# Performance work log

Hardware: AMD Instinct MI355X
Metric: run time of the kernel (lower is better)

Reference implementation:

```python
import jax, jax.numpy as jnp
from jax import lax
import numpy as np

B, C0, C1 = 4, 128, 256
HF = WF = 256
HC = WC = 128
N_CROPS = 2048
WS0, WS1 = 8, 10
PAD0, PAD1 = 0, 1
STRIDE = 8
NW = (WF + 2 * PAD0 - WS0) // STRIDE + 1  # 32 windows per row (same for both crops)


def setup_inputs() -> dict:
    key = jax.random.key(0)
    ks = jax.random.split(key, 16)
    inp = {
        'x0_fine': jax.random.normal(ks[0], (B, C0, HF, WF), jnp.float32),
        'x0_coarse': jax.random.normal(ks[1], (B, C1, HC, WC), jnp.float32),
        'x1_fine': jax.random.normal(ks[2], (B, C0, HF, WF), jnp.float32),
        'x1_coarse': jax.random.normal(ks[3], (B, C1, HC, WC), jnp.float32),
        'proj0_w': jax.random.normal(ks[4], (C1, C0, 1, 1), jnp.float32) * 0.05,
        'proj_last_w': jax.random.normal(ks[5], (C1, C1, 1, 1), jnp.float32) * 0.05,
        'fuse_w1': jax.random.normal(ks[6], (C1, C1, 3, 3), jnp.float32) * 0.02,
        'bn_gamma': jnp.ones((C1,), jnp.float32),
        'bn_beta': jnp.zeros((C1,), jnp.float32),
        'bn_mean': jax.random.normal(ks[7], (C1,), jnp.float32) * 0.1,
        'bn_var': jax.random.uniform(ks[8], (C1,), jnp.float32) + 0.5,
        'fuse_w2': jax.random.normal(ks[9], (C0, C1, 3, 3), jnp.float32) * 0.02,
        'b_idx': jax.random.randint(ks[10], (N_CROPS,), 0, B, jnp.int32),
        'i_idx': jax.random.randint(ks[11], (N_CROPS,), 0, NW * NW, jnp.int32),
        'j_idx': jax.random.randint(ks[12], (N_CROPS,), 0, NW * NW, jnp.int32),
    }
    return inp


def conv2d(x, w, pad):
    return lax.conv_general_dilated(x, w, (1, 1), [(pad, pad), (pad, pad)],
                                    dimension_numbers=('NCHW', 'OIHW', 'NCHW'))


def up2_align_corners(x):
    # bilinear upsample x2 with align_corners=True, separable along H then W
    def interp(x, axis):
        n_in = x.shape[axis]
        n_out = 2 * n_in
        pos = jnp.arange(n_out, dtype=x.dtype) * ((n_in - 1) / (n_out - 1))
        i0 = jnp.clip(jnp.floor(pos).astype(jnp.int32), 0, n_in - 2)
        w = pos - i0.astype(x.dtype)
        a = jnp.take(x, i0, axis=axis)
        b = jnp.take(x, i0 + 1, axis=axis)
        shp = [1] * x.ndim
        shp[axis] = n_out
        w = w.reshape(shp)
        return a * (1 - w) + b * w
    return interp(interp(x, 2), 3)


def fuse(fine, coarse, proj0_w, proj_last_w, fuse_w1, bn_gamma, bn_beta, bn_mean, bn_var, fuse_w2):
    x0 = conv2d(coarse, proj_last_w, 0)                 # projs[-1]
    x0 = conv2d(fine, proj0_w, 0) + up2_align_corners(x0)
    y = conv2d(x0, fuse_w1, 1)
    inv = lax.rsqrt(bn_var + 1e-5)
    y = (y - bn_mean[None, :, None, None]) * (bn_gamma * inv)[None, :, None, None] + bn_beta[None, :, None, None]
    y = jnp.where(y >= 0, y, 0.01 * y)                  # LeakyReLU
    return conv2d(y, fuse_w2, 1)


def crop_windows(x, ws, pad, b, idx):
    # direct sparse window gather; avoids materializing the dense unfold tensor
    xp = jnp.pad(x, ((0, 0), (0, 0), (pad, pad), (pad, pad)))
    nW = (x.shape[3] + 2 * pad - ws) // STRIDE + 1
    r0 = (idx // nW) * STRIDE
    c0 = (idx % nW) * STRIDE
    rows = r0[:, None] + jnp.arange(ws)                 # [n, ws]
    cols = c0[:, None] + jnp.arange(ws)                 # [n, ws]
    crops = xp[b[:, None, None], :, rows[:, :, None], cols[:, None, :]]  # [n, ws, ws, C]
    return jnp.transpose(crops, (0, 3, 1, 2))           # [n, C, ws, ws]


def reference(x0_fine, x0_coarse, x1_fine, x1_coarse, proj0_w, proj_last_w,
              fuse_w1, bn_gamma, bn_beta, bn_mean, bn_var, fuse_w2,
              b_idx, i_idx, j_idx):
    # shapes equal -> concat, fuse once, chunk (matches torch branch)
    fine = jnp.concatenate([x0_fine, x1_fine], 0)
    coarse = jnp.concatenate([x0_coarse, x1_coarse], 0)
    y = fuse(fine, coarse, proj0_w, proj_last_w, fuse_w1, bn_gamma, bn_beta, bn_mean, bn_var, fuse_w2)
    x0, x1 = y[:B], y[B:]
    x0_cropped = crop_windows(x0, WS0, PAD0, b_idx, i_idx)
    x1_cropped = crop_windows(x1, WS1, PAD1, b_idx, j_idx)
    return (x0_cropped, x1_cropped)
```

## Files before the change

kernel.cpp:

```cpp
#include <hip/hip_runtime.h>

typedef __attribute__((ext_vector_type(8))) __bf16 bf16x8;
typedef __attribute__((ext_vector_type(4))) float f32x4;
typedef __attribute__((ext_vector_type(16))) float f32x16;

__device__ __forceinline__ unsigned short fbf(float f) {
  union { float f; unsigned u; } x; x.f = f;
  unsigned r = x.u + 0x7fffu + ((x.u >> 16) & 1u);
  return (unsigned short)(r >> 16);
}
__device__ __forceinline__ float bf2f(unsigned short h) {
  union { unsigned u; float f; } x; x.u = ((unsigned)h) << 16;
  return x.f;
}

#define OFF_WPL 0u
#define OFF_WP0 131072u
#define OFF_WT1 196608u
#define OFF_WT2 1376256u
#define OFF_BNS 1966080u
#define OFF_BNB 1967104u
#define OFF_T1  4194304u
#define OFF_X0  (OFF_T1 + 67108864u)
#define OFF_Y   (OFF_X0 + 268435456u)
#define OFF_YF  OFF_T1

__global__ void prep_kernel(const float* __restrict__ pl, const float* __restrict__ p0,
                            const float* __restrict__ w1, const float* __restrict__ w2,
                            const float* __restrict__ gam, const float* __restrict__ bet,
                            const float* __restrict__ mean, const float* __restrict__ var,
                            unsigned short* __restrict__ wpl, unsigned short* __restrict__ wp0,
                            unsigned short* __restrict__ wt1, unsigned short* __restrict__ wt2,
                            float* __restrict__ bns, float* __restrict__ bnb) {
  int t = blockIdx.x * blockDim.x + threadIdx.x;
  int stride = gridDim.x * blockDim.x;
  for (int i = t; i < 65536; i += stride) wpl[i] = fbf(pl[i]);
  for (int i = t; i < 32768; i += stride) wp0[i] = fbf(p0[i]);
  for (int i = t; i < 589824; i += stride) {
    int e = i & 7, l = (i >> 3) & 63, ks = (i >> 9) & 1;
    int cib = (i >> 10) & 7, cb = (i >> 13) & 7, tap = i >> 16;
    int ci = cib * 32 + ks * 16 + (l >> 5) * 8 + e;
    int co = cb * 32 + (l & 31);
    wt1[i] = fbf(w1[(co * 256 + ci) * 9 + tap]);
  }
  for (int i = t; i < 294912; i += stride) {
    int e = i & 7, l = (i >> 3) & 63, ks = (i >> 9) & 1;
    int cib = (i >> 10) & 7, cb = (i >> 13) & 3, tap = i >> 15;
    int ci = cib * 32 + ks * 16 + (l >> 5) * 8 + e;
    int co = cb * 32 + (l & 31);
    wt2[i] = fbf(w2[(co * 256 + ci) * 9 + tap]);
  }
  for (int i = t; i < 256; i += stride) {
    float s = gam[i] * rsqrtf(var[i] + 1e-5f);
    bns[i] = s; bnb[i] = bet[i] - mean[i] * s;
  }
}

template <int K, int HW, int WD, int EPI>
__global__ __launch_bounds__(512) void gemm1x1_kernel(
    const float* __restrict__ srcA, const float* __restrict__ srcB,
    const unsigned short* __restrict__ wmat,
    unsigned short* __restrict__ outp,
    const unsigned short* __restrict__ t1) {
  __shared__ unsigned short in_lds[128 * 32];
  __shared__ unsigned short w_lds[128 * 32];
  const int tid = threadIdx.x;
  const int pix0 = blockIdx.x * 128;
  const int co0 = blockIdx.y * 128;
  const int n = pix0 / HW;
  const int rem = pix0 % HW;
  const int h = rem / WD;
  const int w0 = rem % WD;
  const float* src = (n < 4) ? (srcA + (size_t)n * K * HW) : (srcB + (size_t)(n - 4) * K * HW);
  const float* rowbase = src + (size_t)h * WD + w0;
  const int wv = tid >> 6, lane = tid & 63;
  const int pw = wv >> 1, cw = wv & 1;
  const int l15 = lane & 15, k8 = lane >> 4;
  f32x4 zero = {0.f, 0.f, 0.f, 0.f};
  f32x4 acc[2][4];
#pragma unroll
  for (int i = 0; i < 2; i++)
#pragma unroll
    for (int j = 0; j < 4; j++) acc[i][j] = zero;
  const int sci = tid >> 4;
  const int sps = (tid & 15) * 8;
  const int wrow = tid >> 2, wsg = tid & 3;
  for (int cib = 0; cib < K / 32; ++cib) {
    int ci0 = cib * 32;
    __syncthreads();
    {
      const float* p = rowbase + (size_t)(ci0 + sci) * HW + sps;
      float4 v0 = *(const float4*)p;
      float4 v1 = *(const float4*)(p + 4);
      float vv[8] = {v0.x, v0.y, v0.z, v0.w, v1.x, v1.y, v1.z, v1.w};
#pragma unroll
      for (int i = 0; i < 8; i++) {
        int row = sps + i;
        int g = (sci >> 3) ^ ((row >> 1) & 3);
        in_lds[row * 32 + g * 8 + (sci & 7)] = fbf(vv[i]);
      }
    }
    {
      int4 v = *(const int4*)&wmat[(size_t)(co0 + wrow) * K + ci0 + wsg * 8];
      *(int4*)&w_lds[wrow * 32 + ((wsg ^ ((wrow >> 1) & 3)) << 3)] = v;
    }
    __syncthreads();
    bf16x8 b[4];
#pragma unroll
    for (int nf = 0; nf < 4; nf++) {
      int row = cw * 64 + nf * 16 + l15;
      b[nf] = *(const bf16x8*)&w_lds[row * 32 + ((k8 ^ ((row >> 1) & 3)) << 3)];
    }
#pragma unroll
    for (int mf = 0; mf < 2; mf++) {
      int row = pw * 32 + mf * 16 + l15;
      bf16x8 a = *(const bf16x8*)&in_lds[row * 32 + ((k8 ^ ((row >> 1) & 3)) << 3)];
#pragma unroll
      for (int nf = 0; nf < 4; nf++)
        acc[mf][nf] = __builtin_amdgcn_mfma_f32_16x16x32_bf16(a, b[nf], acc[mf][nf], 0, 0, 0);
    }
  }
  float fh = 0.f; int i0 = 0;
  if (EPI == 1) {
    float ph = (float)h * (127.0f / 255.0f);
    i0 = (int)ph; if (i0 > 126) i0 = 126;
    fh = ph - (float)i0;
  }
#pragma unroll
  for (int mf = 0; mf < 2; mf++) {
#pragma unroll
    for (int nf = 0; nf < 4; nf++) {
      int co = co0 + cw * 64 + nf * 16 + l15;
#pragma unroll
      for (int r = 0; r < 4; r++) {
        int m = pw * 32 + mf * 16 + k8 * 4 + r;
        float v = acc[mf][nf][r];
        if (EPI == 1) {
          int ww = w0 + m;
          float pww = (float)ww * (127.0f / 255.0f);
          int j0 = (int)pww; if (j0 > 126) j0 = 126;
          float fw = pww - (float)j0;
          const unsigned short* tb = t1 + ((size_t)(n * 128 + i0) * 128 + j0) * 256 + co;
          float a00 = bf2f(tb[0]);
          float a01 = bf2f(tb[256]);
          float a10 = bf2f(tb[128 * 256]);
          float a11 = bf2f(tb[128 * 256 + 256]);
          float top = a00 + fw * (a01 - a00);
          float bot = a10 + fw * (a11 - a10);
          v += top + fh * (bot - top);
        }
        outp[(size_t)(pix0 + m) * 256 + co] = fbf(v);
      }
    }
  }
}

template <int COT, int BNRELU>
__global__ __launch_bounds__(256, 2) void conv3x3_kernel(
    const unsigned short* __restrict__ inp,
    const unsigned short* __restrict__ wtr,
    unsigned short* __restrict__ outp,
    const float* __restrict__ bns, const float* __restrict__ bnb) {
  constexpr int WPT = COT / 32;
  __shared__ unsigned short xl[2][4 * 204 * 8];
  const int tid = threadIdx.x;
  const int bx = blockIdx.x;
  const int n = bx >> 9;
  const int h0 = ((bx >> 3) & 63) * 4;
  const int w0 = (bx & 7) * 32;
  const int co0 = blockIdx.y * 128;
  const int lane = tid & 63, cw = tid >> 6;
  const int l31 = lane & 31, lh = lane >> 5;
  const int cb = (co0 >> 5) + cw;

  f32x16 acc[4];
#pragma unroll
  for (int m = 0; m < 4; m++)
#pragma unroll
    for (int r = 0; r < 16; r++) acc[m][r] = 0.f;

#define FRAG_ADDR(tap, ks, cc) ((((size_t)((tap) * WPT + cb) * 8 + (cc)) * 2 + (ks)) * 512 + lane * 8)

  bf16x8 B[3][3][2];
#pragma unroll
  for (int kh = 0; kh < 3; kh++)
#pragma unroll
    for (int kw = 0; kw < 3; kw++)
#pragma unroll
      for (int ks = 0; ks < 2; ks++)
        B[kh][kw][ks] = *(const bf16x8*)&wtr[FRAG_ADDR(kh * 3 + kw, ks, 0)];

  const size_t nbase = (size_t)n * 256 * 256 * 256;
  for (int s = tid; s < 816; s += 256) {
    int p = s >> 2, g = s & 3;
    int row = p / 34, col = p - row * 34;
    int gh = h0 + row - 1, gw = w0 + col - 1;
    int4 v = make_int4(0, 0, 0, 0);
    if ((unsigned)gh < 256u && (unsigned)gw < 256u)
      v = *(const int4*)&inp[nbase + ((size_t)gh * 256 + gw) * 256 + g * 8];
    *(int4*)&xl[0][(g * 204 + p) * 8] = v;
  }
  __syncthreads();

  for (int cib = 0; cib < 8; ++cib) {
    const int cin = (cib + 1) & 7;
    int4 vr[4]; bool va[4]; int ldst[4];
    if (cib < 7) {
#pragma unroll
      for (int q = 0; q < 4; ++q) {
        int s = tid + q * 256;
        va[q] = s < 816;
        int p = s >> 2, g = s & 3;
        int row = p / 34, col = p - row * 34;
        int gh = h0 + row - 1, gw = w0 + col - 1;
        ldst[q] = (g * 204 + p) * 8;
        vr[q] = make_int4(0, 0, 0, 0);
        if (va[q] && (unsigned)gh < 256u && (unsigned)gw < 256u)
          vr[q] = *(const int4*)&inp[nbase + ((size_t)gh * 256 + gw) * 256 + cin * 32 + g * 8];
      }
    }
    const unsigned short* xb = xl[cib & 1];
    bf16x8 af[2][6];
#pragma unroll
    for (int kw = 0; kw < 3; kw++)
#pragma unroll
      for (int ks = 0; ks < 2; ks++)
        af[0][kw * 2 + ks] = *(const bf16x8*)&xb[((ks * 2 + lh) * 204 + l31 + kw) * 8];
    __builtin_amdgcn_s_setprio(1);
#pragma unroll
    for (int r = 0; r < 6; ++r) {
      const int cur = r & 1, nxt = cur ^ 1;
      if (r < 5) {
#pragma unroll
        for (int kw = 0; kw < 3; kw++)
#pragma unroll
          for (int ks = 0; ks < 2; ks++)
            af[nxt][kw * 2 + ks] =
                *(const bf16x8*)&xb[((ks * 2 + lh) * 204 + (r + 1) * 34 + l31 + kw) * 8];
      }
#pragma unroll
      for (int kw = 0; kw < 3; kw++)
#pragma unroll
        for (int ks = 0; ks < 2; ks++)
#pragma unroll
          for (int kh = 0; kh < 3; kh++) {
            int m = r - kh;
            if (m >= 0 && m < 4)
              acc[m] = __builtin_amdgcn_mfma_f32_32x32x16_bf16(af[cur][kw * 2 + ks],
                                                               B[kh][kw][ks], acc[m], 0, 0, 0);
          }
      if (r >= 3) {
        int kh = r - 3;
#pragma unroll
        for (int kw = 0; kw < 3; ++kw)
#pragma unroll
          for (int ks = 0; ks < 2; ++ks)
            B[kh][kw][ks] = *(const bf16x8*)&wtr[FRAG_ADDR(kh * 3 + kw, ks, cin)];
      }
    }
    __builtin_amdgcn_s_setprio(0);
    if (cib < 7) {
#pragma unroll
      for (int q = 0; q < 4; ++q)
        if (va[q]) *(int4*)&xl[cin & 1][ldst[q]] = vr[q];
      __syncthreads();
    }
  }
#undef FRAG_ADDR

  const int coL = co0 + cw * 32 + l31;
  float s = 1.f, t = 0.f;
  if (BNRELU) { s = bns[coL]; t = bnb[coL]; }
#pragma unroll
  for (int m = 0; m < 4; ++m) {
    int h = h0 + m;
    size_t rowb = (((size_t)(n * 256 + h) * 256) + w0) * COT + coL;
#pragma unroll
    for (int r = 0; r < 16; ++r) {
      int wofs = (r & 3) + 8 * (r >> 2) + 4 * lh;
      float v = acc[m][r];
      if (BNRELU) { v = v * s + t; v = (v >= 0.f) ? v : 0.01f * v; }
      outp[rowb + (size_t)wofs * COT] = fbf(v);
    }
  }
}

template <int WS, int PAD>
__global__ __launch_bounds__(256) void gather_kernel(
    const unsigned short* __restrict__ yf,
    const int* __restrict__ bidx, const int* __restrict__ widx,
    int bofs, float* __restrict__ outp) {
  const int WS2 = WS * WS;
  __shared__ unsigned short tile[WS * WS * 140];
  const int crop = blockIdx.x, tid = threadIdx.x;
  const int b = bidx[crop] + bofs;
  const int idx = widx[crop];
  const int r0 = (idx >> 5) * 8, c0 = (idx & 31) * 8;
  for (int t = tid; t < WS2 * 16; t += 256) {
    int p = t >> 4, sg = t & 15;
    int r = p / WS, cc = p - r * WS;
    int sr = r0 + r - PAD, sc = c0 + cc - PAD;
    int4 v = make_int4(0, 0, 0, 0);
    if ((unsigned)sr < 256u && (unsigned)sc < 256u)
      v = *(const int4*)&yf[(((size_t)(b * 256 + sr) * 256) + sc) * 128 + sg * 8];
    *(int2*)&tile[p * 140 + sg * 8] = make_int2(v.x, v.y);
    *(int2*)&tile[p * 140 + sg * 8 + 4] = make_int2(v.z, v.w);
  }
  __syncthreads();
  float* dst = outp + (size_t)crop * 128 * WS2;
  for (int o = tid; o < 64 * WS2; o += 256) {
    int cp = o / WS2, p = o - cp * WS2;
    unsigned v = *(const unsigned*)&tile[p * 140 + cp * 2];
    dst[(2 * cp) * WS2 + p] = bf2f((unsigned short)(v & 0xffffu));
    dst[(2 * cp + 1) * WS2 + p] = bf2f((unsigned short)(v >> 16));
  }
}

extern "C" void kernel_launch(void* const* d_in, const int* in_sizes, int n_in,
                              void* d_out, int out_size, void* d_ws, size_t ws_size,
                              hipStream_t stream) {
  const float* x0f = (const float*)d_in[0];
  const float* x0c = (const float*)d_in[1];
  const float* x1f = (const float*)d_in[2];
  const float* x1c = (const float*)d_in[3];
  const float* p0w = (const float*)d_in[4];
  const float* plw = (const float*)d_in[5];
  const float* fw1 = (const float*)d_in[6];
  const float* gam = (const float*)d_in[7];
  const float* bet = (const float*)d_in[8];
  const float* men = (const float*)d_in[9];
  const float* var = (const float*)d_in[10];
  const float* fw2 = (const float*)d_in[11];
  const int* b_idx = (const int*)d_in[12];
  const int* i_idx = (const int*)d_in[13];
  const int* j_idx = (const int*)d_in[14];
  (void)in_sizes; (void)n_in; (void)out_size; (void)ws_size;

  char* ws = (char*)d_ws;
  unsigned short* wpl = (unsigned short*)(ws + OFF_WPL);
  unsigned short* wp0 = (unsigned short*)(ws + OFF_WP0);
  unsigned short* wt1 = (unsigned short*)(ws + OFF_WT1);
  unsigned short* wt2 = (unsigned short*)(ws + OFF_WT2);
  float* bns = (float*)(ws + OFF_BNS);
  float* bnb = (float*)(ws + OFF_BNB);
  unsigned short* t1 = (unsigned short*)(ws + OFF_T1);
  unsigned short* x0 = (unsigned short*)(ws + OFF_X0);
  unsigned short* y = (unsigned short*)(ws + OFF_Y);
  unsigned short* yf = (unsigned short*)(ws + OFF_YF);
  float* out0 = (float*)d_out;
  float* out1 = out0 + (size_t)2048 * 128 * 64;

  prep_kernel<<<512, 256, 0, stream>>>(plw, p0w, fw1, fw2, gam, bet, men, var,
                                       wpl, wp0, wt1, wt2, bns, bnb);
  gemm1x1_kernel<256, 16384, 128, 0><<<dim3(1024, 2), 512, 0, stream>>>(x0c, x1c, wpl, t1, nullptr);
  gemm1x1_kernel<128, 65536, 256, 1><<<dim3(4096, 2), 512, 0, stream>>>(x0f, x1f, wp0, x0, t1);
  conv3x3_kernel<256, 1><<<dim3(4096, 2), 256, 0, stream>>>(x0, wt1, y, bns, bnb);
  conv3x3_kernel<128, 0><<<dim3(4096, 1), 256, 0, stream>>>(y, wt2, yf, nullptr, nullptr);
  gather_kernel<8, 0><<<2048, 256, 0, stream>>>(yf, b_idx, i_idx, 0, out0);
  gather_kernel<10, 1><<<2048, 256, 0, stream>>>(yf, b_idx, j_idx, 4, out1);
}
```

Before: 1.215 ms.

## Stage two 32-channel input blocks per LDS buffer to halve conv barriers

The 3x3 conv kernel now loads 64 input channels per pipeline stage, in two 32-channel sub-buffers, instead of 32. This halves the number of __syncthreads and global-load phases, and more loads are in flight per stage. Source pointers are computed once and advanced, which removes the repeated index math. In exchange, LDS use doubles (about 52KB per block), which may limit occupancy, and register pressure from the extra prefetched vectors goes up.

New measurement: 1.359 ms. 1.12x slower.

```diff
diff --git a/kernel.cpp b/kernel.cpp
--- a/kernel.cpp
+++ b/kernel.cpp
@@ -162,7 +162,7 @@
     unsigned short* __restrict__ outp,
     const float* __restrict__ bns, const float* __restrict__ bnb) {
   constexpr int WPT = COT / 32;
-  __shared__ unsigned short xl[2][4 * 204 * 8];
+  __shared__ unsigned short xl[2][2][6528];
   const int tid = threadIdx.x;
   const int bx = blockIdx.x;
   const int n = bx >> 9;
@@ -191,78 +191,101 @@
         B[kh][kw][ks] = *(const bf16x8*)&wtr[FRAG_ADDR(kh * 3 + kw, ks, 0)];
 
   const size_t nbase = (size_t)n * 256 * 256 * 256;
-  for (int s = tid; s < 816; s += 256) {
+  const unsigned short* srcq[4];
+  int ldst[4];
+  bool va[4];
+#pragma unroll
+  for (int q = 0; q < 4; ++q) {
+    int s = tid + q * 256;
+    va[q] = s < 816;
     int p = s >> 2, g = s & 3;
     int row = p / 34, col = p - row * 34;
     int gh = h0 + row - 1, gw = w0 + col - 1;
-    int4 v = make_int4(0, 0, 0, 0);
-    if ((unsigned)gh < 256u && (unsigned)gw < 256u)
-      v = *(const int4*)&inp[nbase + ((size_t)gh * 256 + gw) * 256 + g * 8];
-    *(int4*)&xl[0][(g * 204 + p) * 8] = v;
+    ldst[q] = (g * 204 + p) * 8;
+    bool ok = va[q] && ((unsigned)gh < 256u) && ((unsigned)gw < 256u);
+    srcq[q] = ok ? (inp + nbase + (((size_t)gh * 256 + gw) * 256 + g * 8)) : nullptr;
+  }
+
+#pragma unroll
+  for (int q = 0; q < 4; ++q) {
+    int4 v0 = make_int4(0, 0, 0, 0), v1 = make_int4(0, 0, 0, 0);
+    if (srcq[q]) {
+      v0 = *(const int4*)srcq[q];
+      v1 = *(const int4*)(srcq[q] + 32);
+      srcq[q] += 64;
+    }
+    if (va[q]) {
+      *(int4*)&xl[0][0][ldst[q]] = v0;
+      *(int4*)&xl[0][1][ldst[q]] = v1;
+    }
   }
   __syncthreads();
 
-  for (int cib = 0; cib < 8; ++cib) {
-    const int cin = (cib + 1) & 7;
-    int4 vr[4]; bool va[4]; int ldst[4];
-    if (cib < 7) {
+  for (int ii = 0; ii < 4; ++ii) {
+    int4 vr[4][2];
+    if (ii < 3) {
 #pragma unroll
       for (int q = 0; q < 4; ++q) {
-        int s = tid + q * 256;
-        va[q] = s < 816;
-        int p = s >> 2, g = s & 3;
-        int row = p / 34, col = p - row * 34;
-        int gh = h0 + row - 1, gw = w0 + col - 1;
-        ldst[q] = (g * 204 + p) * 8;
-        vr[q] = make_int4(0, 0, 0, 0);
-        if (va[q] && (unsigned)gh < 256u && (unsigned)gw < 256u)
-          vr[q] = *(const int4*)&inp[nbase + ((size_t)gh * 256 + gw) * 256 + cin * 32 + g * 8];
+        vr[q][0] = make_int4(0, 0, 0, 0);
+        vr[q][1] = make_int4(0, 0, 0, 0);
+        if (srcq[q]) {
+          vr[q][0] = *(const int4*)srcq[q];
+          vr[q][1] = *(const int4*)(srcq[q] + 32);
+          srcq[q] += 64;
+        }
       }
     }
-    const unsigned short* xb = xl[cib & 1];
-    bf16x8 af[2][6];
-#pragma unroll
-    for (int kw = 0; kw < 3; kw++)
-#pragma unroll
-      for (int ks = 0; ks < 2; ks++)
-        af[0][kw * 2 + ks] = *(const bf16x8*)&xb[((ks * 2 + lh) * 204 + l31 + kw) * 8];
-    __builtin_amdgcn_s_setprio(1);
-#pragma unroll
-    for (int r = 0; r < 6; ++r) {
-      const int cur = r & 1, nxt = cur ^ 1;
-      if (r < 5) {
+#pragma unroll
+    for (int sub = 0; sub < 2; ++sub) {
+      const unsigned short* xb = xl[ii & 1][sub];
+      const int tgt = ii * 2 + 1 + sub;
+      bf16x8 af[2][6];
+#pragma unroll
+      for (int kw = 0; kw < 3; kw++)
+#pragma unroll
+        for (int ks = 0; ks < 2; ks++)
+          af[0][kw * 2 + ks] = *(const bf16x8*)&xb[((ks * 2 + lh) * 204 + l31 + kw) * 8];
+      __builtin_amdgcn_s_setprio(1);
+#pragma unroll
+      for (int r = 0; r < 6; ++r) {
+        const int cur = r & 1, nxt = cur ^ 1;
+        if (r < 5) {
+#pragma unroll
+          for (int kw = 0; kw < 3; kw++)
+#pragma unroll
+            for (int ks = 0; ks < 2; ks++)
+              af[nxt][kw * 2 + ks] =
+                  *(const bf16x8*)&xb[((ks * 2 + lh) * 204 + (r + 1) * 34 + l31 + kw) * 8];
+        }
 #pragma unroll
         for (int kw = 0; kw < 3; kw++)
 #pragma unroll
           for (int ks = 0; ks < 2; ks++)
-            af[nxt][kw * 2 + ks] =
-                *(const bf16x8*)&xb[((ks * 2 + lh) * 204 + (r + 1) * 34 + l31 + kw) * 8];
+#pragma unroll
+            for (int kh = 0; kh < 3; kh++) {
+              int m = r - kh;
+              if (m >= 0 && m < 4)
+                acc[m] = __builtin_amdgcn_mfma_f32_32x32x16_bf16(af[cur][kw * 2 + ks],
+                                                                 B[kh][kw][ks], acc[m], 0, 0, 0);
+            }
+        if (r >= 3 && tgt < 8) {
+          int kh = r - 3;
+#pragma unroll
+          for (int kw = 0; kw < 3; ++kw)
+#pragma unroll
+            for (int ks = 0; ks < 2; ++ks)
+              B[kh][kw][ks] = *(const bf16x8*)&wtr[FRAG_ADDR(kh * 3 + kw, ks, tgt)];
+        }
       }
-#pragma unroll
-      for (int kw = 0; kw < 3; kw++)
-#pragma unroll
-        for (int ks = 0; ks < 2; ks++)
-#pragma unroll
-          for (int kh = 0; kh < 3; kh++) {
-            int m = r - kh;
-            if (m >= 0 && m < 4)
-              acc[m] = __builtin_amdgcn_mfma_f32_32x32x16_bf16(af[cur][kw * 2 + ks],
-                                                               B[kh][kw][ks], acc[m], 0, 0, 0);
-          }
-      if (r >= 3) {
-        int kh = r - 3;
-#pragma unroll
-        for (int kw = 0; kw < 3; ++kw)
-#pragma unroll
-          for (int ks = 0; ks < 2; ++ks)
-            B[kh][kw][ks] = *(const bf16x8*)&wtr[FRAG_ADDR(kh * 3 + kw, ks, cin)];
-      }
-    }
-    __builtin_amdgcn_s_setprio(0);
-    if (cib < 7) {
+      __builtin_amdgcn_s_setprio(0);
+    }
+    if (ii < 3) {
 #pragma unroll
       for (int q = 0; q < 4; ++q)
-        if (va[q]) *(int4*)&xl[cin & 1][ldst[q]] = vr[q];
+        if (va[q]) {
+          *(int4*)&xl[(ii + 1) & 1][0][ldst[q]] = vr[q][0];
+          *(int4*)&xl[(ii + 1) & 1][1][ldst[q]] = vr[q][1];
+        }
       __syncthreads();
     }
   }
```

## Use padded channel-grouped layout so conv3x3 reads operands directly from global

Applied to the files above, without the earlier changes.

Intermediate activations are stored in a padded layout grouped by channel, with zeroed border columns and a zero buffer for out-of-range rows. The 3x3 conv kernels now load MFMA A-fragments straight from global/L2 instead of staging tiles through LDS, and blocks are remapped so the two output-channel halves and neighbouring tiles run close together. This removes LDS staging and bounds checks but depends on cache hits for the repeated overlapping reads, and it drops the occupancy hint from the launch bounds. An extra kernel zeroes the padding.

Result: slower. 1.581 ms (+30.1%).

```diff
diff --git a/kernel.cpp b/kernel.cpp
--- a/kernel.cpp
+++ b/kernel.cpp
@@ -20,10 +20,11 @@
 #define OFF_WT2 1376256u
 #define OFF_BNS 1966080u
 #define OFF_BNB 1967104u
-#define OFF_T1  4194304u
-#define OFF_X0  (OFF_T1 + 67108864u)
-#define OFF_Y   (OFF_X0 + 268435456u)
-#define OFF_YF  OFF_T1
+#define OFF_ZG  1968128u
+#define OFF_X0G 4194304u
+#define OFF_YG  (OFF_X0G + 270532608u)
+#define OFF_T1  OFF_YG
+#define OFF_YF  OFF_X0G
 
 __global__ void prep_kernel(const float* __restrict__ pl, const float* __restrict__ p0,
                             const float* __restrict__ w1, const float* __restrict__ w2,
@@ -31,7 +32,9 @@
                             const float* __restrict__ mean, const float* __restrict__ var,
                             unsigned short* __restrict__ wpl, unsigned short* __restrict__ wp0,
                             unsigned short* __restrict__ wt1, unsigned short* __restrict__ wt2,
-                            float* __restrict__ bns, float* __restrict__ bnb) {
+                            float* __restrict__ bns, float* __restrict__ bnb,
+                            int* __restrict__ zg,
+                            unsigned short* __restrict__ x0g) {
   int t = blockIdx.x * blockDim.x + threadIdx.x;
   int stride = gridDim.x * blockDim.x;
   for (int i = t; i < 65536; i += stride) wpl[i] = fbf(pl[i]);
@@ -50,9 +53,25 @@
     int co = cb * 32 + (l & 31);
     wt2[i] = fbf(w2[(co * 256 + ci) * 9 + tap]);
   }
+  for (int i = t; i < 1024; i += stride) zg[i] = 0;
+  for (int i = t; i < 1048576; i += stride) {
+    int e = i & 7, wsel = (i >> 3) & 1, g = (i >> 4) & 31, nh = i >> 9;
+    size_t a = (((size_t)nh * 32 + g) * 258 + (wsel ? 257 : 0)) * 8 + e;
+    x0g[a] = 0;
+  }
   for (int i = t; i < 256; i += stride) {
     float s = gam[i] * rsqrtf(var[i] + 1e-5f);
     bns[i] = s; bnb[i] = bet[i] - mean[i] * s;
+  }
+}
+
+__global__ void padzero_kernel(unsigned short* __restrict__ yg) {
+  int t = blockIdx.x * blockDim.x + threadIdx.x;
+  int stride = gridDim.x * blockDim.x;
+  for (int i = t; i < 1048576; i += stride) {
+    int e = i & 7, wsel = (i >> 3) & 1, g = (i >> 4) & 31, nh = i >> 9;
+    size_t a = (((size_t)nh * 32 + g) * 258 + (wsel ? 257 : 0)) * 8 + e;
+    yg[a] = 0;
   }
 }
 
@@ -148,27 +167,38 @@
           float top = a00 + fw * (a01 - a00);
           float bot = a10 + fw * (a11 - a10);
           v += top + fh * (bot - top);
+          size_t a = ((((size_t)(n * 256 + h) * 32) + (co >> 3)) * 258 + (ww + 1)) * 8 + (co & 7);
+          outp[a] = fbf(v);
+        } else {
+          outp[(size_t)(pix0 + m) * 256 + co] = fbf(v);
         }
-        outp[(size_t)(pix0 + m) * 256 + co] = fbf(v);
-      }
-    }
-  }
-}
-
-template <int COT, int BNRELU>
-__global__ __launch_bounds__(256, 2) void conv3x3_kernel(
-    const unsigned short* __restrict__ inp,
+      }
+    }
+  }
+}
+
+template <int COT, int BNRELU, int NCO, int OUTG>
+__global__ __launch_bounds__(256) void conv3x3_kernel(
+    const unsigned short* __restrict__ xg,
     const unsigned short* __restrict__ wtr,
     unsigned short* __restrict__ outp,
-    const float* __restrict__ bns, const float* __restrict__ bnb) {
+    const float* __restrict__ bns, const float* __restrict__ bnb,
+    const unsigned short* __restrict__ zg) {
   constexpr int WPT = COT / 32;
-  __shared__ unsigned short xl[2][4 * 204 * 8];
   const int tid = threadIdx.x;
   const int bx = blockIdx.x;
-  const int n = bx >> 9;
-  const int h0 = ((bx >> 3) & 63) * 4;
-  const int w0 = (bx & 7) * 32;
-  const int co0 = blockIdx.y * 128;
+  int q, co0;
+  if (NCO == 2) {
+    int xs = bx & 7, t = bx >> 3;
+    co0 = (t & 1) * 128;
+    q = (t >> 1) * 8 + xs;
+  } else {
+    co0 = 0;
+    q = (bx & 7) * 512 + (bx >> 3);
+  }
+  const int n = q >> 9;
+  const int h0 = ((q >> 3) & 63) * 4;
+  const int w0 = (q & 7) * 32;
   const int lane = tid & 63, cw = tid >> 6;
   const int l31 = lane & 31, lh = lane >> 5;
   const int cb = (co0 >> 5) + cw;
@@ -190,53 +220,42 @@
       for (int ks = 0; ks < 2; ks++)
         B[kh][kw][ks] = *(const bf16x8*)&wtr[FRAG_ADDR(kh * 3 + kw, ks, 0)];
 
-  const size_t nbase = (size_t)n * 256 * 256 * 256;
-  for (int s = tid; s < 816; s += 256) {
-    int p = s >> 2, g = s & 3;
-    int row = p / 34, col = p - row * 34;
-    int gh = h0 + row - 1, gw = w0 + col - 1;
-    int4 v = make_int4(0, 0, 0, 0);
-    if ((unsigned)gh < 256u && (unsigned)gw < 256u)
-      v = *(const int4*)&inp[nbase + ((size_t)gh * 256 + gw) * 256 + g * 8];
-    *(int4*)&xl[0][(g * 204 + p) * 8] = v;
-  }
-  __syncthreads();
-
+  const unsigned short* bas[6][2];
+  int dr[6];
+#pragma unroll
+  for (int r = 0; r < 6; ++r) {
+    int gh = h0 + r - 1;
+    bool ok = (unsigned)gh < 256u;
+    dr[r] = ok ? 8256 : 0;
+#pragma unroll
+    for (int ks = 0; ks < 2; ++ks)
+      bas[r][ks] = ok ? xg + ((((size_t)(n * 256 + gh) * 32) + (ks * 2 + lh)) * 258 + (w0 + l31)) * 8
+                      : zg + l31 * 8;
+  }
+
+  bf16x8 af[2][6];
+  auto loadrow = [&](bf16x8* dst, int rr) {
+#pragma unroll
+    for (int kw = 0; kw < 3; ++kw)
+#pragma unroll
+      for (int ks = 0; ks < 2; ++ks)
+        dst[kw * 2 + ks] = *(const bf16x8*)(bas[rr][ks] + kw * 8);
+  };
+
+  loadrow(af[0], 0);
   for (int cib = 0; cib < 8; ++cib) {
-    const int cin = (cib + 1) & 7;
-    int4 vr[4]; bool va[4]; int ldst[4];
-    if (cib < 7) {
-#pragma unroll
-      for (int q = 0; q < 4; ++q) {
-        int s = tid + q * 256;
-        va[q] = s < 816;
-        int p = s >> 2, g = s & 3;
-        int row = p / 34, col = p - row * 34;
-        int gh = h0 + row - 1, gw = w0 + col - 1;
-        ldst[q] = (g * 204 + p) * 8;
-        vr[q] = make_int4(0, 0, 0, 0);
-        if (va[q] && (unsigned)gh < 256u && (unsigned)gw < 256u)
-          vr[q] = *(const int4*)&inp[nbase + ((size_t)gh * 256 + gw) * 256 + cin * 32 + g * 8];
-      }
-    }
-    const unsigned short* xb = xl[cib & 1];
-    bf16x8 af[2][6];
-#pragma unroll
-    for (int kw = 0; kw < 3; kw++)
-#pragma unroll
-      for (int ks = 0; ks < 2; ks++)
-        af[0][kw * 2 + ks] = *(const bf16x8*)&xb[((ks * 2 + lh) * 204 + l31 + kw) * 8];
     __builtin_amdgcn_s_setprio(1);
 #pragma unroll
     for (int r = 0; r < 6; ++r) {
       const int cur = r & 1, nxt = cur ^ 1;
       if (r < 5) {
-#pragma unroll
-        for (int kw = 0; kw < 3; kw++)
-#pragma unroll
-          for (int ks = 0; ks < 2; ks++)
-            af[nxt][kw * 2 + ks] =
-                *(const bf16x8*)&xb[((ks * 2 + lh) * 204 + (r + 1) * 34 + l31 + kw) * 8];
+        loadrow(af[nxt], r + 1);
+      } else if (cib < 7) {
+#pragma unroll
+        for (int rr = 0; rr < 6; ++rr)
+#pragma unroll
+          for (int ks = 0; ks < 2; ++ks) bas[rr][ks] += dr[rr];
+        loadrow(af[nxt], 0);
       }
 #pragma unroll
       for (int kw = 0; kw < 3; kw++)
@@ -249,22 +268,17 @@
               acc[m] = __builtin_amdgcn_mfma_f32_32x32x16_bf16(af[cur][kw * 2 + ks],
                                                                B[kh][kw][ks], acc[m], 0, 0, 0);
           }
-      if (r >= 3) {
+      if (r >= 3 && cib < 7) {
         int kh = r - 3;
 #pragma unroll
         for (int kw = 0; kw < 3; ++kw)
 #pragma unroll
           for (int ks = 0; ks < 2; ++ks)
-            B[kh][kw][ks] = *(const bf16x8*)&wtr[FRAG_ADDR(kh * 3 + kw, ks, cin)];
+            B[kh][kw][ks] = *(const bf16x8*)&wtr[FRAG_ADDR(kh * 3 + kw, ks, cib + 1)];
       }
     }
     __builtin_amdgcn_s_setprio(0);
-    if (cib < 7) {
-#pragma unroll
-      for (int q = 0; q < 4; ++q)
-        if (va[q]) *(int4*)&xl[cin & 1][ldst[q]] = vr[q];
-      __syncthreads();
-    }
+    if (cib < 7) asm volatile("s_barrier" ::: "memory");
   }
 #undef FRAG_ADDR
 
@@ -274,13 +288,17 @@
 #pragma unroll
   for (int m = 0; m < 4; ++m) {
     int h = h0 + m;
-    size_t rowb = (((size_t)(n * 256 + h) * 256) + w0) * COT + coL;
 #pragma unroll
     for (int r = 0; r < 16; ++r) {
       int wofs = (r & 3) + 8 * (r >> 2) + 4 * lh;
       float v = acc[m][r];
       if (BNRELU) { v = v * s + t; v = (v >= 0.f) ? v : 0.01f * v; }
-      outp[rowb + (size_t)wofs * COT] = fbf(v);
+      if (OUTG) {
+        size_t a = ((((size_t)(n * 256 + h) * 32) + (coL >> 3)) * 258 + (w0 + wofs + 1)) * 8 + (coL & 7);
+        outp[a] = fbf(v);
+      } else {
+        outp[(((size_t)(n * 256 + h) * 256) + w0 + wofs) * COT + coL] = fbf(v);
+      }
     }
   }
 }
@@ -343,19 +361,21 @@
   unsigned short* wt2 = (unsigned short*)(ws + OFF_WT2);
   float* bns = (float*)(ws + OFF_BNS);
   float* bnb = (float*)(ws + OFF_BNB);
+  unsigned short* zg = (unsigned short*)(ws + OFF_ZG);
+  unsigned short* x0g = (unsigned short*)(ws + OFF_X0G);
+  unsigned short* yg = (unsigned short*)(ws + OFF_YG);
   unsigned short* t1 = (unsigned short*)(ws + OFF_T1);
-  unsigned short* x0 = (unsigned short*)(ws + OFF_X0);
-  unsigned short* y = (unsigned short*)(ws + OFF_Y);
   unsigned short* yf = (unsigned short*)(ws + OFF_YF);
   float* out0 = (float*)d_out;
   float* out1 = out0 + (size_t)2048 * 128 * 64;
 
   prep_kernel<<<512, 256, 0, stream>>>(plw, p0w, fw1, fw2, gam, bet, men, var,
-                                       wpl, wp0, wt1, wt2, bns, bnb);
+                                       wpl, wp0, wt1, wt2, bns, bnb, (int*)zg, x0g);
   gemm1x1_kernel<256, 16384, 128, 0><<<dim3(1024, 2), 512, 0, stream>>>(x0c, x1c, wpl, t1, nullptr);
-  gemm1x1_kernel<128, 65536, 256, 1><<<dim3(4096, 2), 512, 0, stream>>>(x0f, x1f, wp0, x0, t1);
-  conv3x3_kernel<256, 1><<<dim3(4096, 2), 256, 0, stream>>>(x0, wt1, y, bns, bnb);
-  conv3x3_kernel<128, 0><<<dim3(4096, 1), 256, 0, stream>>>(y, wt2, yf, nullptr, nullptr);
+  gemm1x1_kernel<128, 65536, 256, 1><<<dim3(4096, 2), 512, 0, stream>>>(x0f, x1f, wp0, x0g, t1);
+  padzero_kernel<<<512, 256, 0, stream>>>(yg);
+  conv3x3_kernel<256, 1, 2, 1><<<dim3(8192), 256, 0, stream>>>(x0g, wt1, yg, bns, bnb, zg);
+  conv3x3_kernel<128, 0, 1, 0><<<dim3(4096), 256, 0, stream>>>(yg, wt2, yf, bns, bnb, zg);
   gather_kernel<8, 0><<<2048, 256, 0, stream>>>(yf, b_idx, i_idx, 0, out0);
   gather_kernel<10, 1><<<2048, 256, 0, stream>>>(yf, b_idx, j_idx, 4, out1);
 }
```
